# Optimization experiments

Measured on AMD Instinct MI355X. Metric: run time of the kernel, lower is better.

## Reference

```python
import jax, jax.numpy as jnp
import numpy as np

B, N, C_IN, T = 16, 1024, 16, 36
K, C_OUT = 3, 64


def setup_inputs() -> dict:
    key = jax.random.key(0)
    k1, k2, k3, k4 = jax.random.split(key, 4)
    x = jax.random.normal(k1, (B, N, C_IN, T), dtype=jnp.float32)
    spatial_attention = jax.random.uniform(k2, (B, N, N), dtype=jnp.float32)
    cheb = jax.random.normal(k3, (K, N, N), dtype=jnp.float32) * 0.1
    theta = jax.random.normal(k4, (K, C_IN, C_OUT), dtype=jnp.float32) * 0.1
    return {"x": x, "spatial_attention": spatial_attention, "cheb": cheb, "theta": theta}


def reference(x, spatial_attention, cheb, theta):
    # x: [B,N,C_in,T], spatial_attention: [B,N,N], cheb: [K,N,N], theta: [K,C_in,C_out]
    # Original: per (t,k): ((T_k * SAt).T @ x[..., t]) @ theta_k, summed over k, ReLU.
    # Compute attention-weighted adjacency ONCE (time-invariant), batch over all t.
    t_at = cheb[:, None, :, :] * spatial_attention[None]          # [K,B,N,N]
    # rhs[k,b,n,c,t] = sum_m t_at[k,b,m,n] * x[b,m,c,t]  (permute(0,2,1).matmul)
    rhs = jnp.einsum('kbmn,bmct->kbnct', t_at, x)                 # [K,B,N,C_in,T]
    out = jnp.einsum('kbnct,kco->bnot', rhs, theta)               # [B,N,C_out,T]
    return jax.nn.relu(out)
```

## Files before the change

### kernel.cpp

```cpp
#include <hip/hip_runtime.h>
#include <hip/hip_bf16.h>

#define NB 16
#define NN 1024
#define CIN 16
#define TT 36
#define KK 3
#define COUT 64
#define CT 576
#define KB 48

typedef __attribute__((ext_vector_type(8))) short bf16x8;
typedef __attribute__((ext_vector_type(4))) float f32x4;

__device__ __forceinline__ unsigned short f2bf(float f) {
    union { float f; unsigned int u; } v; v.f = f;
    unsigned int r = v.u + 0x7FFF + ((v.u >> 16) & 1);
    return (unsigned short)(r >> 16);
}

__global__ __launch_bounds__(256) void prep_both(const float* __restrict__ cheb,
                                                 const float* __restrict__ sat,
                                                 ushort* __restrict__ At,
                                                 const float* __restrict__ x,
                                                 ushort* __restrict__ Xt,
                                                 int n_base, int rows, int na_blocks) {
    __shared__ ushort tile[64][68];
    const int tid = threadIdx.x;
    const int bid = blockIdx.x;

    if (bid < na_blocks) {
        const int ntiles = rows >> 6;
        const int per_k = ntiles * 16;
        const int k = bid / per_k;
        const int bx = bid - k * per_k;
        const int n0 = n_base + (bx % ntiles) * 64;
        const int m0 = (bx / ntiles) * 64;

        size_t goff[4];
        float4 cv[4], sv[4];
#pragma unroll
        for (int i = 0; i < 4; ++i) {
            int f = i * 256 + tid;
            goff[i] = (size_t)(m0 + (f >> 4)) * NN + n0 + ((f & 15) << 2);
            cv[i] = *(const float4*)(cheb + (size_t)k * NN * NN + goff[i]);
            sv[i] = *(const float4*)(sat + goff[i]);
        }
        for (int b = 0; b < 16; ++b) {
#pragma unroll
            for (int i = 0; i < 4; ++i) {
                int f = i * 256 + tid;
                ushort4 u;
                u.x = f2bf(cv[i].x * sv[i].x); u.y = f2bf(cv[i].y * sv[i].y);
                u.z = f2bf(cv[i].z * sv[i].z); u.w = f2bf(cv[i].w * sv[i].w);
                *(ushort4*)&tile[f >> 4][(f & 15) << 2] = u;
            }
            if (b < 15) {
                const float* sa = sat + (size_t)(b + 1) * NN * NN;
#pragma unroll
                for (int i = 0; i < 4; ++i) sv[i] = *(const float4*)(sa + goff[i]);
            }
            __syncthreads();
            ushort* outp = At + (size_t)(k * 16 + b) * rows * NN;
#pragma unroll
            for (int i = 0; i < 4; ++i) {
                int f = i * 256 + tid;
                int n = f >> 4, m4 = (f & 15) << 2;
                ushort4 u;
                u.x = tile[m4 + 0][n]; u.y = tile[m4 + 1][n];
                u.z = tile[m4 + 2][n]; u.w = tile[m4 + 3][n];
                *(ushort4*)(outp + (size_t)(n0 - n_base + n) * NN + m0 + m4) = u;
            }
            __syncthreads();
        }
    } else {
        const int f0 = bid - na_blocks;
        const int b = f0 / 144;
        const int bx = f0 - b * 144;
        const int m0 = (bx & 15) * 64;
        const int c0 = (bx >> 4) * 64;
        const float* xb = x + (size_t)b * NN * CT;
#pragma unroll
        for (int i = 0; i < 4; ++i) {
            int f = i * 256 + tid;
            int mr = f >> 4, c4 = (f & 15) << 2;
            float4 v = *(const float4*)(xb + (size_t)(m0 + mr) * CT + c0 + c4);
            ushort4 u;
            u.x = f2bf(v.x); u.y = f2bf(v.y); u.z = f2bf(v.z); u.w = f2bf(v.w);
            *(ushort4*)&tile[mr][c4] = u;
        }
        __syncthreads();
        ushort* outp = Xt + (size_t)b * CT * NN;
#pragma unroll
        for (int i = 0; i < 4; ++i) {
            int f = i * 256 + tid;
            int n = f >> 4, m4 = (f & 15) << 2;
            int ctlin = c0 + n;
            int c = ctlin / 36, t = ctlin - 36 * c;
            int ctp = t * 16 + c;
            ushort4 u;
            u.x = tile[m4 + 0][n]; u.y = tile[m4 + 1][n];
            u.z = tile[m4 + 2][n]; u.w = tile[m4 + 3][n];
            *(ushort4*)(outp + (size_t)ctp * NN + m0 + m4) = u;
        }
    }
}

__global__ __launch_bounds__(512) void gemm1(const ushort* __restrict__ At,
                                             const ushort* __restrict__ Xt,
                                             ushort* __restrict__ rhs2,
                                             int nsplit, int n_base, int rows) {
    __shared__ ushort lds[3 * 384 * 64];
    const int tid = threadIdx.x;
    const int b = blockIdx.y;
    const int ntiles = rows >> 6;
    const int nt = blockIdx.x % ntiles;
    const int ctt = blockIdx.x / ntiles;
    const int nloc0 = nt * 64;
    const int ct0 = ctt * 192;
    const int atrows = nsplit ? rows : NN;

    const int srow = tid >> 3, schunk = tid & 7;
    const int swz = schunk ^ (srow & 7);
    const ushort* a_src[3];
#pragma unroll
    for (int k = 0; k < 3; ++k)
        a_src[k] = At + ((size_t)(k * 16 + b) * atrows + nloc0 + srow) * NN + swz * 8;
    const ushort* b_src = Xt + (size_t)b * CT * NN + (size_t)(ct0 + srow) * NN + swz * 8;

    auto STAGE = [&](int kt, int p) {
        const int mk = kt * 64;
        ushort* base = lds + p * (384 * 64);
#pragma unroll
        for (int k = 0; k < 3; ++k)
            __builtin_amdgcn_global_load_lds(
                (const __attribute__((address_space(1))) void*)(a_src[k] + mk),
                (__attribute__((address_space(3))) void*)(base + k * 4096 + tid * 8), 16, 0, 0);
#pragma unroll
        for (int i = 0; i < 3; ++i)
            __builtin_amdgcn_global_load_lds(
                (const __attribute__((address_space(1))) void*)(b_src + (size_t)i * 64 * NN + mk),
                (__attribute__((address_space(3))) void*)(base + 3 * 4096 + (tid + i * 512) * 8), 16, 0, 0);
    };

    const int w = tid >> 6, lane = tid & 63;
    const int wr = w >> 2, wc = w & 3;
    const int lrow = lane & 15, quad = lane >> 4;
    const int s3 = lrow & 7;
    f32x4 acc[3][2][3] = {};

    STAGE(0, 0);
    STAGE(1, 1);
    asm volatile("s_waitcnt vmcnt(6)\n\ts_barrier" ::: "memory");

    for (int kt = 0; kt < 16; ++kt) {
        if (kt + 2 < 16)
            STAGE(kt + 2, (kt + 2) % 3);
        const ushort* bufA = lds + (kt % 3) * (384 * 64);
        const ushort* bufB = bufA + 3 * 4096;
#pragma unroll
        for (int kp = 0; kp < 2; ++kp) {
            const int koff = (((kp * 4 + quad) ^ s3) << 3);
            bf16x8 af[3][2], bfr[3];
#pragma unroll
            for (int k = 0; k < 3; ++k)
#pragma unroll
                for (int mi = 0; mi < 2; ++mi)
                    af[k][mi] = *(const bf16x8*)&bufA[k * 4096 + (wr * 32 + mi * 16 + lrow) * 64 + koff];
#pragma unroll
            for (int ni = 0; ni < 3; ++ni)
                bfr[ni] = *(const bf16x8*)&bufB[(wc * 48 + ni * 16 + lrow) * 64 + koff];
            __builtin_amdgcn_s_setprio(1);
#pragma unroll
            for (int k = 0; k < 3; ++k)
#pragma unroll
                for (int mi = 0; mi < 2; ++mi)
#pragma unroll
                    for (int ni = 0; ni < 3; ++ni)
                        acc[k][mi][ni] = __builtin_amdgcn_mfma_f32_16x16x32_bf16(
                            af[k][mi], bfr[ni], acc[k][mi][ni], 0, 0, 0);
            __builtin_amdgcn_s_setprio(0);
        }
        if (kt + 2 < 16)
            asm volatile("s_waitcnt vmcnt(6)\n\ts_barrier" ::: "memory");
        else if (kt + 1 < 16)
            asm volatile("s_waitcnt vmcnt(0)\n\ts_barrier" ::: "memory");
        else
            asm volatile("s_barrier" ::: "memory");
    }

    ushort* sc = lds + w * 4608;
#pragma unroll
    for (int k = 0; k < 3; ++k)
#pragma unroll
        for (int mi = 0; mi < 2; ++mi)
#pragma unroll
            for (int ni = 0; ni < 3; ++ni)
#pragma unroll
                for (int r = 0; r < 4; ++r)
                    sc[((mi * 16 + quad * 4 + r) * 3 + ni) * 48 + k * 16 + lrow] =
                        f2bf(acc[k][mi][ni][r]);
    asm volatile("s_waitcnt lgkmcnt(0)" ::: "memory");
    const int n_g0 = n_base + nloc0 + wr * 32;
    const int t_g0 = ctt * 12 + wc * 3;
#pragma unroll
    for (int i = 0; i < 9; ++i) {
        int seg = i * 64 + lane;
        int off = seg * 8;
        int nl = off / 144;
        int rem = off - nl * 144;
        int tl = rem / 48, kcol = rem - tl * 48;
        size_t g = (((size_t)b * NN + n_g0 + nl) * 36 + (t_g0 + tl)) * 48 + kcol;
        *(uint4*)(rhs2 + g) = *(const uint4*)&sc[off];
    }
}

__global__ __launch_bounds__(256) void apply_mfma2(const ushort* __restrict__ rhs2,
                                                   const float* __restrict__ theta,
                                                   float* __restrict__ out) {
    __shared__ ushort thT[64 * 72];
    __shared__ float ostage[4][64 * 36];
    const int tid = threadIdx.x;
    for (int f = tid; f < 64 * 64; f += 256) {
        int o = f >> 6, kc = f & 63;
        thT[o * 72 + kc] = f2bf((kc < 48) ? theta[kc * 64 + o] : 0.f);
    }
    __syncthreads();
    const int w = tid >> 6, lane = tid & 63;
    const int lrow = lane & 15, quad = lane >> 4;

    bf16x8 a[4][2];
#pragma unroll
    for (int mi = 0; mi < 4; ++mi)
#pragma unroll
        for (int kc = 0; kc < 2; ++kc)
            a[mi][kc] = *(const bf16x8*)&thT[(mi * 16 + lrow) * 72 + kc * 32 + quad * 8];

    float* ost = &ostage[w][0];
    for (int j = 0; j < 4; ++j) {
        const int bn = blockIdx.x * 16 + w * 4 + j;
        const ushort* rrow = rhs2 + (size_t)bn * (36 * 48);
        f32x4 acc[4][3] = {};
#pragma unroll
        for (int ni = 0; ni < 3; ++ni)
#pragma unroll
            for (int kc = 0; kc < 2; ++kc) {
                bf16x8 bf = *(const bf16x8*)(rrow + (ni * 16 + lrow) * 48 + kc * 32 + quad * 8);
#pragma unroll
                for (int mi = 0; mi < 4; ++mi)
                    acc[mi][ni] = __builtin_amdgcn_mfma_f32_16x16x32_bf16(
                        a[mi][kc], bf, acc[mi][ni], 0, 0, 0);
            }
#pragma unroll
        for (int mi = 0; mi < 4; ++mi)
#pragma unroll
            for (int ni = 0; ni < 3; ++ni)
#pragma unroll
                for (int r = 0; r < 4; ++r) {
                    int t = ni * 16 + lrow;
                    if (t < 36)
                        ost[(mi * 16 + quad * 4 + r) * 36 + t] = fmaxf(acc[mi][ni][r], 0.f);
                }
        asm volatile("s_waitcnt lgkmcnt(0)" ::: "memory");
        float* ob = out + (size_t)bn * (COUT * TT);
#pragma unroll
        for (int q = 0; q < 9; ++q) {
            int f = q * 64 + lane;
            *(float4*)&ob[f * 4] = *(const float4*)&ost[f * 4];
        }
    }
}

__global__ __launch_bounds__(256) void naive_fused(const float* __restrict__ x,
                                                   const float* __restrict__ sat,
                                                   const float* __restrict__ cheb,
                                                   const float* __restrict__ theta,
                                                   float* __restrict__ out) {
    __shared__ float wgt[3][1024];
    __shared__ float rs[3][576];
    const int tid = threadIdx.x;
    const int n = blockIdx.x, b = blockIdx.y;
    for (int f = tid; f < 3 * 1024; f += 256) {
        int k = f >> 10, m = f & 1023;
        wgt[k][m] = cheb[(size_t)k * NN * NN + (size_t)m * NN + n] *
                    sat[(size_t)b * NN * NN + (size_t)m * NN + n];
    }
    __syncthreads();
    float a0[3] = {}, a1[3] = {}, a2[3] = {};
    const float* xb = x + (size_t)b * NN * CT;
    for (int m = 0; m < 1024; ++m) {
        const float* xr = xb + (size_t)m * CT;
        float x0 = xr[tid];
        float x1 = xr[256 + tid];
        float x2 = (tid < 64) ? xr[512 + tid] : 0.f;
#pragma unroll
        for (int k = 0; k < 3; ++k) {
            float wm = wgt[k][m];
            a0[k] += wm * x0; a1[k] += wm * x1; a2[k] += wm * x2;
        }
    }
#pragma unroll
    for (int k = 0; k < 3; ++k) {
        rs[k][tid] = a0[k];
        rs[k][256 + tid] = a1[k];
        if (tid < 64) rs[k][512 + tid] = a2[k];
    }
    __syncthreads();
    const int o = tid >> 2, tg = tid & 3;
    float oa[9] = {};
    for (int kc = 0; kc < 48; ++kc) {
        int k = kc >> 4, c = kc & 15;
        float th = theta[kc * 64 + o];
        const float* rp = &rs[k][c * TT + tg * 9];
#pragma unroll
        for (int j = 0; j < 9; ++j) oa[j] += th * rp[j];
    }
    float* ob = out + ((size_t)b * NN + n) * (COUT * TT);
#pragma unroll
    for (int j = 0; j < 9; ++j)
        ob[o * TT + tg * 9 + j] = fmaxf(oa[j], 0.f);
}

extern "C" void kernel_launch(void* const* d_in, const int* in_sizes, int n_in,
                              void* d_out, int out_size, void* d_ws, size_t ws_size,
                              hipStream_t stream) {
    const float* x     = (const float*)d_in[0];
    const float* sat   = (const float*)d_in[1];
    const float* cheb  = (const float*)d_in[2];
    const float* theta = (const float*)d_in[3];
    float* out = (float*)d_out;

    const size_t RHS2 = (size_t)NB * NN * 36 * 48;
    const size_t XT   = (size_t)NB * CT * NN;
    const size_t ATF  = (size_t)KB * NN * NN;
    const size_t ATNS = (size_t)KB * 512 * NN;
    const size_t needA     = (RHS2 + XT + ATF) * 2;
    const size_t needSplit = (RHS2 + XT + ATNS) * 2;

    ushort* rhs2 = (ushort*)d_ws;
    ushort* Xt   = rhs2 + RHS2;
    ushort* At   = Xt + XT;

    if (ws_size >= needA) {
        prep_both<<<dim3(768 + 2304), 256, 0, stream>>>(cheb, sat, At, x, Xt, 0, 1024, 768);
        gemm1<<<dim3(48, NB), 512, 0, stream>>>(At, Xt, rhs2, 0, 0, 1024);
        apply_mfma2<<<dim3(NB * NN / 16), 256, 0, stream>>>(rhs2, theta, out);
    } else if (ws_size >= needSplit) {
        for (int half = 0; half < 2; ++half) {
            int nb = half * 512;
            int na = 384;
            int grid = na + (half == 0 ? 2304 : 0);
            prep_both<<<dim3(grid), 256, 0, stream>>>(cheb, sat, At, x, Xt, nb, 512, na);
            gemm1<<<dim3(24, NB), 512, 0, stream>>>(At, Xt, rhs2, 1, nb, 512);
        }
        apply_mfma2<<<dim3(NB * NN / 16), 256, 0, stream>>>(rhs2, theta, out);
    } else {
        naive_fused<<<dim3(NN, NB), 256, 0, stream>>>(x, sat, cheb, theta, out);
    }
}
```

Before: 373.6 us.

## Halve gemm1 K-tile to 32 and shrink LDS for two blocks per CU

The gemm1 K-step drops from 64 to 32, which halves the triple-buffered LDS footprint and doubles the main-loop trip count. The staging is rewritten so each thread issues three 16-byte global_load_lds copies with a new 4-chunk XOR swizzle, and the vmcnt waits are adjusted to match. Launch bounds now request 4 waves per SIMD, so two 512-thread blocks can share a CU. In exchange there are twice as many barriers per K, and the register cap may cause spills of the 18 accumulators.

```diff
diff --git a/kernel.cpp b/kernel.cpp
--- a/kernel.cpp
+++ b/kernel.cpp
@@ -106,11 +106,11 @@
     }
 }
 
-__global__ __launch_bounds__(512) void gemm1(const ushort* __restrict__ At,
-                                             const ushort* __restrict__ Xt,
-                                             ushort* __restrict__ rhs2,
-                                             int nsplit, int n_base, int rows) {
-    __shared__ ushort lds[3 * 384 * 64];
+__global__ __launch_bounds__(512, 4) void gemm1(const ushort* __restrict__ At,
+                                                const ushort* __restrict__ Xt,
+                                                ushort* __restrict__ rhs2,
+                                                int nsplit, int n_base, int rows) {
+    __shared__ ushort lds[3 * 384 * 32];
     const int tid = threadIdx.x;
     const int b = blockIdx.y;
     const int ntiles = rows >> 6;
@@ -120,70 +120,77 @@
     const int ct0 = ctt * 192;
     const int atrows = nsplit ? rows : NN;
 
-    const int srow = tid >> 3, schunk = tid & 7;
-    const int swz = schunk ^ (srow & 7);
-    const ushort* a_src[3];
-#pragma unroll
-    for (int k = 0; k < 3; ++k)
-        a_src[k] = At + ((size_t)(k * 16 + b) * atrows + nloc0 + srow) * NN + swz * 8;
-    const ushort* b_src = Xt + (size_t)b * CT * NN + (size_t)(ct0 + srow) * NN + swz * 8;
+    const ushort* AtB = At + (size_t)b * atrows * NN;
+    const ushort* XtB = Xt + (size_t)b * CT * NN + (size_t)ct0 * NN;
+
+    size_t srcoff[3];
+#pragma unroll
+    for (int i = 0; i < 3; ++i) {
+        int s = i * 512 + tid;
+        if (s < 768) {
+            int k = s >> 8, rr = (s >> 2) & 63, cc = s & 3;
+            int cs = cc ^ ((rr >> 1) & 3);
+            srcoff[i] = (size_t)(k * 16) * atrows * NN + (size_t)(nloc0 + rr) * NN + cs * 8;
+        } else {
+            int sb = s - 768;
+            int rr = sb >> 2, cc = sb & 3;
+            int cs = cc ^ ((rr >> 1) & 3);
+            srcoff[i] = (size_t)rr * NN + cs * 8;
+        }
+    }
+    const bool isA0 = (tid < 512);
+    auto SRC = [&](int i, int mk) -> const ushort* {
+        int s = i * 512 + tid;
+        const ushort* base = (s < 768) ? AtB : XtB;
+        return base + srcoff[i] + mk;
+    };
 
     auto STAGE = [&](int kt, int p) {
-        const int mk = kt * 64;
-        ushort* base = lds + p * (384 * 64);
-#pragma unroll
-        for (int k = 0; k < 3; ++k)
-            __builtin_amdgcn_global_load_lds(
-                (const __attribute__((address_space(1))) void*)(a_src[k] + mk),
-                (__attribute__((address_space(3))) void*)(base + k * 4096 + tid * 8), 16, 0, 0);
+        const int mk = kt * 32;
+        ushort* base = lds + p * 12288;
 #pragma unroll
         for (int i = 0; i < 3; ++i)
             __builtin_amdgcn_global_load_lds(
-                (const __attribute__((address_space(1))) void*)(b_src + (size_t)i * 64 * NN + mk),
-                (__attribute__((address_space(3))) void*)(base + 3 * 4096 + (tid + i * 512) * 8), 16, 0, 0);
+                (const __attribute__((address_space(1))) void*)SRC(i, mk),
+                (__attribute__((address_space(3))) void*)(base + (tid + i * 512) * 8), 16, 0, 0);
     };
 
     const int w = tid >> 6, lane = tid & 63;
     const int wr = w >> 2, wc = w & 3;
     const int lrow = lane & 15, quad = lane >> 4;
-    const int s3 = lrow & 7;
+    const int koff = ((quad ^ ((lrow >> 1) & 3)) << 3);
     f32x4 acc[3][2][3] = {};
 
     STAGE(0, 0);
     STAGE(1, 1);
-    asm volatile("s_waitcnt vmcnt(6)\n\ts_barrier" ::: "memory");
-
-    for (int kt = 0; kt < 16; ++kt) {
-        if (kt + 2 < 16)
+    asm volatile("s_waitcnt vmcnt(3)\n\ts_barrier" ::: "memory");
+
+    for (int kt = 0; kt < 32; ++kt) {
+        if (kt + 2 < 32)
             STAGE(kt + 2, (kt + 2) % 3);
-        const ushort* bufA = lds + (kt % 3) * (384 * 64);
-        const ushort* bufB = bufA + 3 * 4096;
-#pragma unroll
-        for (int kp = 0; kp < 2; ++kp) {
-            const int koff = (((kp * 4 + quad) ^ s3) << 3);
-            bf16x8 af[3][2], bfr[3];
-#pragma unroll
-            for (int k = 0; k < 3; ++k)
-#pragma unroll
-                for (int mi = 0; mi < 2; ++mi)
-                    af[k][mi] = *(const bf16x8*)&bufA[k * 4096 + (wr * 32 + mi * 16 + lrow) * 64 + koff];
-#pragma unroll
-            for (int ni = 0; ni < 3; ++ni)
-                bfr[ni] = *(const bf16x8*)&bufB[(wc * 48 + ni * 16 + lrow) * 64 + koff];
-            __builtin_amdgcn_s_setprio(1);
-#pragma unroll
-            for (int k = 0; k < 3; ++k)
-#pragma unroll
-                for (int mi = 0; mi < 2; ++mi)
-#pragma unroll
-                    for (int ni = 0; ni < 3; ++ni)
-                        acc[k][mi][ni] = __builtin_amdgcn_mfma_f32_16x16x32_bf16(
-                            af[k][mi], bfr[ni], acc[k][mi][ni], 0, 0, 0);
-            __builtin_amdgcn_s_setprio(0);
-        }
-        if (kt + 2 < 16)
-            asm volatile("s_waitcnt vmcnt(6)\n\ts_barrier" ::: "memory");
-        else if (kt + 1 < 16)
+        const ushort* buf = lds + (kt % 3) * 12288;
+        bf16x8 af[3][2], bfr[3];
+#pragma unroll
+        for (int k = 0; k < 3; ++k)
+#pragma unroll
+            for (int mi = 0; mi < 2; ++mi)
+                af[k][mi] = *(const bf16x8*)&buf[k * 2048 + (wr * 32 + mi * 16 + lrow) * 32 + koff];
+#pragma unroll
+        for (int ni = 0; ni < 3; ++ni)
+            bfr[ni] = *(const bf16x8*)&buf[6144 + (wc * 48 + ni * 16 + lrow) * 32 + koff];
+        __builtin_amdgcn_s_setprio(1);
+#pragma unroll
+        for (int k = 0; k < 3; ++k)
+#pragma unroll
+            for (int mi = 0; mi < 2; ++mi)
+#pragma unroll
+                for (int ni = 0; ni < 3; ++ni)
+                    acc[k][mi][ni] = __builtin_amdgcn_mfma_f32_16x16x32_bf16(
+                        af[k][mi], bfr[ni], acc[k][mi][ni], 0, 0, 0);
+        __builtin_amdgcn_s_setprio(0);
+        if (kt + 2 < 32)
+            asm volatile("s_waitcnt vmcnt(3)\n\ts_barrier" ::: "memory");
+        else if (kt + 1 < 32)
             asm volatile("s_waitcnt vmcnt(0)\n\ts_barrier" ::: "memory");
         else
             asm volatile("s_barrier" ::: "memory");
```

After: 369.8 us. Within noise of the previous version (-1.0%).
